# Performance work log

Measured on AMD Instinct MI355X. Metric: run time of the kernel, lower is better.

## Reference

```python
import jax, jax.numpy as jnp
import numpy as np

N = 40000
E = 640000
D = 256
H = 8
DH = D // H
DFF = 4 * D
SCALE = D ** (-0.5)
EPS = 1e-5


def layernorm(x, g, b):
    mu = jnp.mean(x, axis=-1, keepdims=True)
    var = jnp.mean(jnp.square(x - mu), axis=-1, keepdims=True)
    return (x - mu) * jax.lax.rsqrt(var + EPS) * g + b


def setup_inputs() -> dict:
    key = jax.random.key(0)
    ks = jax.random.split(key, 12)
    inv = 1.0 / np.sqrt(D)
    invf = 1.0 / np.sqrt(DFF)
    return {
        "triplet_h": jax.random.normal(ks[0], (N, D), dtype=jnp.float32),
        "src": jax.random.randint(ks[1], (E,), 0, N, dtype=jnp.int32),
        "dst": jax.random.randint(ks[2], (E,), 0, N, dtype=jnp.int32),
        "Wqkv": jax.random.uniform(ks[3], (D, 3 * D), jnp.float32, -inv, inv),
        "bqkv": jax.random.uniform(ks[4], (3 * D,), jnp.float32, -inv, inv),
        "ln_attn_g": jnp.ones((D,), jnp.float32),
        "ln_attn_b": jnp.zeros((D,), jnp.float32),
        "ln_res_g": jnp.ones((D,), jnp.float32),
        "ln_res_b": jnp.zeros((D,), jnp.float32),
        "W_in": jax.random.uniform(ks[5], (D, DFF), jnp.float32, -inv, inv),
        "b_in": jax.random.uniform(ks[6], (DFF,), jnp.float32, -inv, inv),
        "W_out": jax.random.uniform(ks[7], (DFF, D), jnp.float32, -invf, invf),
        "b_out": jax.random.uniform(ks[8], (D,), jnp.float32, -invf, invf),
    }


def reference(triplet_h, src, dst, Wqkv, bqkv, ln_attn_g, ln_attn_b,
              ln_res_g, ln_res_b, W_in, b_in, W_out, b_out):
    n = triplet_h.shape[0]
    h = layernorm(triplet_h, ln_attn_g, ln_attn_b)
    qkv = (h @ Wqkv + bqkv).reshape(n, 3, H, DH)
    q = qkv[:, 0] * SCALE          # [N, H, DH]
    k = qkv[:, 1]
    v = qkv[:, 2]

    # per-edge attention logits: dot(Q_src, K_dst) per head -> [E, H]
    scores = jnp.einsum('ehd,ehd->eh', q[src], k[dst])
    # segment softmax over incoming edges of each dst node
    m = jax.ops.segment_max(scores, dst, num_segments=n)      # [N, H]
    e = jnp.exp(scores - m[dst])
    s = jax.ops.segment_sum(e, dst, num_segments=n)           # [N, H]
    sa = e / s[dst]                                           # [E, H]

    # weighted scatter-sum of src V into dst nodes
    he = (v[src] * sa[:, :, None]).reshape(-1, D)             # [E, D]
    agg = jax.ops.segment_sum(he, dst, num_segments=n)        # [N, D]

    # Residual block: x = triplet_h + agg; x + MLP(LN(x))
    x = triplet_h + agg
    y = layernorm(x, ln_res_g, ln_res_b)
    y = jax.nn.gelu(y @ W_in + b_in, approximate=False) @ W_out + b_out
    return x + y
```

## Files before the change

kernel.cpp:

```cpp
#include <hip/hip_runtime.h>
#include <math.h>

#define N_NODES 40000
#define M_PAD   40064
#define N_EDGES 640000
#define D       256
#define H       8
#define DFF     1024
#define D3      768
#define ATT_SCALE 0.0625f
#define LN_EPS  1e-5f

typedef __attribute__((ext_vector_type(8))) short short8;
typedef __attribute__((ext_vector_type(4))) float f32x4;
typedef __attribute__((ext_vector_type(2))) float f32x2;

__device__ __forceinline__ unsigned short f2bf(float f) {
    unsigned int u = __builtin_bit_cast(unsigned int, f);
    u = (u + 0x7FFF + ((u >> 16) & 1)) >> 16;
    return (unsigned short)u;
}
__device__ __forceinline__ float bf2f(unsigned short u) {
    return __builtin_bit_cast(float, (unsigned int)u << 16);
}

__device__ __forceinline__ float fast_gelu(float x) {
    const float z  = fabsf(x) * 0.70710678118654752f;
    const float t  = __builtin_amdgcn_rcpf(1.0f + 0.3275911f * z);
    float p = 1.061405429f;
    p = p * t - 1.453152027f;
    p = p * t + 1.421413741f;
    p = p * t - 0.284496736f;
    p = p * t + 0.254829592f;
    const float e  = __expf(-z * z);
    const float ea = 1.0f - p * t * e;
    const float er = (x < 0.0f) ? -ea : ea;
    return 0.5f * x * (1.0f + er);
}

#define GLOAD_LDS16(g, l) \
    __builtin_amdgcn_global_load_lds((const __attribute__((address_space(1))) void*)(g), \
                                     (__attribute__((address_space(3))) void*)(l), 16, 0, 0)

#if __has_builtin(__builtin_amdgcn_cvt_pk_fp8_f32) && __has_builtin(__builtin_amdgcn_cvt_pk_f32_fp8)
#define HW_FP8 1
#else
#define HW_FP8 0
__device__ __forceinline__ unsigned char enc_e4m3(float f) {
    unsigned int u = __builtin_bit_cast(unsigned int, f);
    unsigned int s = (u >> 24) & 0x80;
    float a = fabsf(f);
    if (a >= 0x1p-6f) {
        unsigned int bits = __builtin_bit_cast(unsigned int, a);
        unsigned int q = bits >> 20;
        unsigned int rem = bits & 0xFFFFFu;
        q += (rem > 0x80000u) || ((rem == 0x80000u) && (q & 1));
        q -= 960;
        if (q > 126) q = 126;
        return (unsigned char)(s | q);
    }
    float t = a * 512.0f;
    unsigned int r = (unsigned int)rintf(t);
    return (unsigned char)(s | r);
}
__device__ __forceinline__ float dec_e4m3(unsigned int v) {
    unsigned int em = v & 0x7f;
    float n = __builtin_bit_cast(float, (em << 20) + 0x3C000000u);
    float r = (em >= 8) ? n : (float)em * 0x1p-9f;
    return (v & 0x80) ? -r : r;
}
#endif

__device__ __forceinline__ unsigned int pack4_e4m3(float a, float b, float c, float d) {
#if HW_FP8
    unsigned int w = (unsigned int)__builtin_amdgcn_cvt_pk_fp8_f32(a, b, 0, false);
    w = (unsigned int)__builtin_amdgcn_cvt_pk_fp8_f32(c, d, (int)w, true);
    return w;
#else
    return (unsigned int)enc_e4m3(a) | ((unsigned int)enc_e4m3(b) << 8)
         | ((unsigned int)enc_e4m3(c) << 16) | ((unsigned int)enc_e4m3(d) << 24);
#endif
}
__device__ __forceinline__ void dec4_e4m3(unsigned int w, float& a, float& b, float& c, float& d) {
#if HW_FP8
    f32x2 lo = __builtin_amdgcn_cvt_pk_f32_fp8((int)w, false);
    f32x2 hi = __builtin_amdgcn_cvt_pk_f32_fp8((int)w, true);
    a = lo[0]; b = lo[1]; c = hi[0]; d = hi[1];
#else
    a = dec_e4m3(w & 0xff); b = dec_e4m3((w >> 8) & 0xff);
    c = dec_e4m3((w >> 16) & 0xff); d = dec_e4m3(w >> 24);
#endif
}

#define NB_LN   (M_PAD / 4)
#define NB_PACK 352
#define NB_HIST (N_EDGES / 256)

__device__ __forceinline__ void ln_body(const float* __restrict__ in,
                                        const float* __restrict__ g,
                                        const float* __restrict__ b,
                                        unsigned short* __restrict__ out, int blk)
{
    const int row  = blk * 4 + (threadIdx.x >> 6);
    const int lane = threadIdx.x & 63;
    const size_t off = (((size_t)(row >> 4) * (D / 8) + (lane >> 1)) * 16 + (row & 15)) * 8
                       + (lane & 1) * 4;
    if (row >= N_NODES) {
        ushort4 z = {0, 0, 0, 0};
        *reinterpret_cast<ushort4*>(out + off) = z;
        return;
    }
    const float4 v = *reinterpret_cast<const float4*>(in + (size_t)row * D + lane * 4);
    float s  = v.x + v.y + v.z + v.w;
    float s2 = v.x * v.x + v.y * v.y + v.z * v.z + v.w * v.w;
#pragma unroll
    for (int o = 32; o > 0; o >>= 1) {
        s  += __shfl_xor(s,  o, 64);
        s2 += __shfl_xor(s2, o, 64);
    }
    const float mu  = s * (1.0f / D);
    const float var = s2 * (1.0f / D) - mu * mu;
    const float rs  = rsqrtf(var + LN_EPS);
    const float4 gg = *reinterpret_cast<const float4*>(g + lane * 4);
    const float4 bb = *reinterpret_cast<const float4*>(b + lane * 4);
    ushort4 o4;
    o4.x = f2bf((v.x - mu) * rs * gg.x + bb.x);
    o4.y = f2bf((v.y - mu) * rs * gg.y + bb.y);
    o4.z = f2bf((v.z - mu) * rs * gg.z + bb.z);
    o4.w = f2bf((v.w - mu) * rs * gg.w + bb.w);
    *reinterpret_cast<ushort4*>(out + off) = o4;
}

template <int K, int N>
__device__ __forceinline__ void pack_body(const float* __restrict__ W,
                                          unsigned short* __restrict__ Wpk, int blk)
{
    const int idx = blk * 256 + threadIdx.x;
    const int ni  = idx & 15;
    const int kc  = (idx >> 4) % (K / 8);
    const int nt  = idx / (16 * (K / 8));
    const int n   = nt * 16 + ni;
    unsigned short o[8];
#pragma unroll
    for (int i = 0; i < 8; ++i)
        o[i] = f2bf(W[(size_t)(kc * 8 + i) * N + n]);
    *reinterpret_cast<short8*>(Wpk + (size_t)idx * 8) = *reinterpret_cast<short8*>(o);
}

__global__ __launch_bounds__(256) void prep_kernel(const float* __restrict__ triplet_h,
                                                   const float* __restrict__ ln_g,
                                                   const float* __restrict__ ln_b,
                                                   unsigned short* __restrict__ h_xn,
                                                   const float* __restrict__ Wqkv,
                                                   const float* __restrict__ W_in,
                                                   const float* __restrict__ W_out,
                                                   unsigned short* __restrict__ pq,
                                                   unsigned short* __restrict__ pi,
                                                   unsigned short* __restrict__ po,
                                                   const int* __restrict__ dst,
                                                   int* __restrict__ counts)
{
    const int b = blockIdx.x;
    if (b < NB_LN) {
        ln_body(triplet_h, ln_g, ln_b, h_xn, b);
    } else if (b < NB_LN + NB_PACK) {
        const int pb = b - NB_LN;
        if (pb < 96)       pack_body<D, D3 >(Wqkv, pq, pb);
        else if (pb < 224) pack_body<D, DFF>(W_in, pi, pb - 96);
        else               pack_body<DFF, D>(W_out, po, pb - 224);
    } else {
        const int i = (b - NB_LN - NB_PACK) * 256 + threadIdx.x;
        atomicAdd(&counts[dst[i]], 1);
    }
}

template <int EPI, int K, int N>
__global__ __launch_bounds__(256, 4) void mfma_gemm_kernel(const unsigned short* __restrict__ A,
                                                           const unsigned short* __restrict__ Bpk,
                                                           const float* __restrict__ bias,
                                                           void* __restrict__ Cout,
                                                           void* __restrict__ Cout2,
                                                           void* __restrict__ Cout3,
                                                           const float* __restrict__ Xadd)
{
    constexpr int C = N / 128;
    constexpr int P = M_PAD / 128;

    const int bid = blockIdx.x;
    const int xcd = bid & 7;
    const int t   = bid >> 3;
    const int c   = t % C;
    const int p   = (t / C) * 8 + xcd;
    if (p >= P) return;

    __shared__ unsigned short As[4096];
    __shared__ unsigned short Bs[4096];

    const int tid  = threadIdx.x;
    const int wave = tid >> 6;
    const int lane = tid & 63;
    const int row0 = p * 128;
    const int col0 = c * 128;
    const int wm   = (wave >> 1) * 64;
    const int wn   = (wave & 1) * 64;
    const int g    = lane >> 4;
    const int q    = lane & 15;

    f32x4 acc[4][4] = {};

    const int fragoff = g * 128 + q * 8;

    for (int k0 = 0; k0 < K; k0 += 32) {
        const int kq = k0 >> 3;
#pragma unroll
        for (int cc = 0; cc < 2; ++cc) {
            const int mt = wave * 2 + cc;
            const unsigned short* gA =
                A + ((size_t)(row0 / 16 + mt) * (K / 8) + kq) * 128 + lane * 8;
            GLOAD_LDS16(gA, &As[mt * 512]);
            const unsigned short* gB =
                Bpk + ((size_t)(col0 / 16 + mt) * (K / 8) + kq) * 128 + lane * 8;
            GLOAD_LDS16(gB, &Bs[mt * 512]);
        }
        __syncthreads();

        short8 af[4], bf[4];
#pragma unroll
        for (int i = 0; i < 4; ++i) {
            af[i] = *reinterpret_cast<const short8*>(&As[(wm / 16 + i) * 512 + fragoff]);
            bf[i] = *reinterpret_cast<const short8*>(&Bs[(wn / 16 + i) * 512 + fragoff]);
        }
#pragma unroll
        for (int i = 0; i < 4; ++i)
#pragma unroll
            for (int j = 0; j < 4; ++j)
                acc[i][j] = __builtin_amdgcn_mfma_f32_16x16x32_bf16(bf[j], af[i], acc[i][j], 0, 0, 0);
        __syncthreads();
    }

    if constexpr (EPI == 0) {
        if (col0 < 256) {
            unsigned char* q8 = (unsigned char*)Cout;
#pragma unroll
            for (int j = 0; j < 4; ++j) {
                const int nb = col0 + wn + j * 16 + g * 4;
                const float4 bz = *reinterpret_cast<const float4*>(bias + nb);
#pragma unroll
                for (int i = 0; i < 4; ++i) {
                    const int r = row0 + wm + i * 16 + q;
                    if (r >= N_NODES) continue;
                    const unsigned int w = pack4_e4m3(acc[i][j][0] + bz.x, acc[i][j][1] + bz.y,
                                                      acc[i][j][2] + bz.z, acc[i][j][3] + bz.w);
                    *reinterpret_cast<unsigned int*>(q8 + (size_t)r * 256 + nb) = w;
                }
            }
        } else if (col0 < 512) {
            unsigned short* kb = (unsigned short*)Cout2;
#pragma unroll
            for (int j = 0; j < 4; ++j) {
                const int nb = col0 + wn + j * 16 + g * 4;
                const float4 bz = *reinterpret_cast<const float4*>(bias + nb);
#pragma unroll
                for (int i = 0; i < 4; ++i) {
                    const int r = row0 + wm + i * 16 + q;
                    if (r >= N_NODES) continue;
                    ushort4 u;
                    u.x = f2bf(acc[i][j][0] + bz.x);
                    u.y = f2bf(acc[i][j][1] + bz.y);
                    u.z = f2bf(acc[i][j][2] + bz.z);
                    u.w = f2bf(acc[i][j][3] + bz.w);
                    *reinterpret_cast<ushort4*>(kb + (size_t)r * 256 + (nb - 256)) = u;
                }
            }
        } else {
            unsigned char* v8 = (unsigned char*)Cout3;
#pragma unroll
            for (int j = 0; j < 4; ++j) {
                const int nb = col0 + wn + j * 16 + g * 4;
                const float4 bz = *reinterpret_cast<const float4*>(bias + nb);
#pragma unroll
                for (int i = 0; i < 4; ++i) {
                    const int r = row0 + wm + i * 16 + q;
                    if (r >= N_NODES) continue;
                    const unsigned int w = pack4_e4m3(acc[i][j][0] + bz.x, acc[i][j][1] + bz.y,
                                                      acc[i][j][2] + bz.z, acc[i][j][3] + bz.w);
                    *reinterpret_cast<unsigned int*>(v8 + (size_t)r * 256 + (nb - 512)) = w;
                }
            }
        }
    } else if constexpr (EPI == 1) {
#pragma unroll
        for (int j = 0; j < 4; ++j) {
            const int nb = col0 + wn + j * 16 + g * 4;
            const float4 bz = *reinterpret_cast<const float4*>(bias + nb);
#pragma unroll
            for (int i = 0; i < 4; ++i) {
                const int r = row0 + wm + i * 16 + q;
                const float o0 = fast_gelu(acc[i][j][0] + bz.x);
                const float o1 = fast_gelu(acc[i][j][1] + bz.y);
                const float o2 = fast_gelu(acc[i][j][2] + bz.z);
                const float o3 = fast_gelu(acc[i][j][3] + bz.w);
                const size_t off = (((size_t)(r >> 4) * (N / 8) + (nb >> 3)) * 16
                                    + (r & 15)) * 8 + (nb & 7);
                ushort4 u;
                u.x = f2bf(o0); u.y = f2bf(o1); u.z = f2bf(o2); u.w = f2bf(o3);
                *reinterpret_cast<ushort4*>((unsigned short*)Cout + off) = u;
            }
        }
    } else {
#pragma unroll
        for (int j = 0; j < 4; ++j) {
            const int nb = col0 + wn + j * 16 + g * 4;
            const float4 bz = *reinterpret_cast<const float4*>(bias + nb);
#pragma unroll
            for (int i = 0; i < 4; ++i) {
                const int r = row0 + wm + i * 16 + q;
                if (r >= N_NODES) continue;
                const f32x4 xd = __builtin_nontemporal_load(
                    reinterpret_cast<const f32x4*>(Xadd + (size_t)r * N + nb));
                f32x4 ov;
                ov[0] = acc[i][j][0] + bz.x + xd[0];
                ov[1] = acc[i][j][1] + bz.y + xd[1];
                ov[2] = acc[i][j][2] + bz.z + xd[2];
                ov[3] = acc[i][j][3] + bz.w + xd[3];
                __builtin_nontemporal_store(ov,
                    reinterpret_cast<f32x4*>((float*)Cout + (size_t)r * N + nb));
            }
        }
    }
}

__global__ __launch_bounds__(1024) void scan_kernel(const int* __restrict__ counts,
                                                    int* __restrict__ rowptr,
                                                    int* __restrict__ cursor)
{
    const int PER = 40;
    const int tid  = threadIdx.x;
    const int base = tid * PER;
    const bool act = (base < N_NODES);
    int s = 0;
    if (act) {
#pragma unroll
        for (int i = 0; i < PER / 4; ++i) {
            const int4 c4 = *reinterpret_cast<const int4*>(counts + base + i * 4);
            s += (c4.x + c4.y) + (c4.z + c4.w);
        }
    }
    __shared__ int sm[1024];
    sm[tid] = s;
    __syncthreads();
    for (int off = 1; off < 1024; off <<= 1) {
        int t = (tid >= off) ? sm[tid - off] : 0;
        __syncthreads();
        sm[tid] += t;
        __syncthreads();
    }
    int run = sm[tid] - s;
    if (act) {
#pragma unroll
        for (int i = 0; i < PER / 4; ++i) {
            const int4 c4 = *reinterpret_cast<const int4*>(counts + base + i * 4);
            int4 r4;
            r4.x = run;
            r4.y = r4.x + c4.x;
            r4.z = r4.y + c4.y;
            r4.w = r4.z + c4.z;
            run  = r4.w + c4.w;
            *reinterpret_cast<int4*>(rowptr + base + i * 4) = r4;
            *reinterpret_cast<int4*>(cursor + base + i * 4) = r4;
        }
    }
    if (tid == 1023) rowptr[N_NODES] = sm[1023];
}

__global__ __launch_bounds__(256) void fill_kernel(const int* __restrict__ src,
                                                   const int* __restrict__ dst,
                                                   int* __restrict__ cursor,
                                                   int* __restrict__ srcs)
{
    const int e = blockIdx.x * 256 + threadIdx.x;
    const int pos = atomicAdd(&cursor[dst[e]], 1);
    if (pos >= 0 && pos < N_EDGES) srcs[pos] = src[e];
}

__global__ __launch_bounds__(256) void fused_attn_kernel(const unsigned char* __restrict__ qf8,
                                                         const unsigned short* __restrict__ kbf,
                                                         const unsigned char* __restrict__ vf8,
                                                         const int* __restrict__ srcs,
                                                         const int* __restrict__ rowptr,
                                                         const float* __restrict__ triplet_h,
                                                         const float* __restrict__ g,
                                                         const float* __restrict__ b,
                                                         float* __restrict__ x,
                                                         unsigned short* __restrict__ xn)
{
    const int node = blockIdx.x * 4 + (threadIdx.x >> 6);
    const int lane = threadIdx.x & 63;
    int beg = rowptr[node];
    int end = rowptr[node + 1];
    beg = max(0, min(beg, N_EDGES));
    end = max(beg, min(end, N_EDGES));
    const int deg = end - beg;

    const ushort4 ku = *reinterpret_cast<const ushort4*>(
        kbf + (size_t)node * 256 + lane * 4);
    const float k0 = bf2f(ku.x) * ATT_SCALE, k1 = bf2f(ku.y) * ATT_SCALE;
    const float k2 = bf2f(ku.z) * ATT_SCALE, k3 = bf2f(ku.w) * ATT_SCALE;

    float dsum = 0.0f;
    float4 acc = {0.0f, 0.0f, 0.0f, 0.0f};

    for (int base = 0; base < deg; base += 64) {
        const int cnt = min(64, deg - base);
        const int idx = base + lane;
        const int sv = (idx < deg) ? srcs[beg + idx] : 0;
        int j = 0;
        for (; j + 4 <= cnt; j += 4) {
            const int s0 = __builtin_amdgcn_readlane(sv, j);
            const int s1 = __builtin_amdgcn_readlane(sv, j + 1);
            const int s2 = __builtin_amdgcn_readlane(sv, j + 2);
            const int s3 = __builtin_amdgcn_readlane(sv, j + 3);
            const unsigned int qa = *reinterpret_cast<const unsigned int*>(qf8 + (size_t)s0 * 256 + lane * 4);
            const unsigned int qb = *reinterpret_cast<const unsigned int*>(qf8 + (size_t)s1 * 256 + lane * 4);
            const unsigned int qc = *reinterpret_cast<const unsigned int*>(qf8 + (size_t)s2 * 256 + lane * 4);
            const unsigned int qd = *reinterpret_cast<const unsigned int*>(qf8 + (size_t)s3 * 256 + lane * 4);
            const unsigned int va = *reinterpret_cast<const unsigned int*>(vf8 + (size_t)s0 * 256 + lane * 4);
            const unsigned int vb = *reinterpret_cast<const unsigned int*>(vf8 + (size_t)s1 * 256 + lane * 4);
            const unsigned int vc = *reinterpret_cast<const unsigned int*>(vf8 + (size_t)s2 * 256 + lane * 4);
            const unsigned int vd = *reinterpret_cast<const unsigned int*>(vf8 + (size_t)s3 * 256 + lane * 4);
            float a0, a1, a2, a3;
            dec4_e4m3(qa, a0, a1, a2, a3);
            float p0 = a0 * k0 + a1 * k1 + a2 * k2 + a3 * k3;
            dec4_e4m3(qb, a0, a1, a2, a3);
            float p1 = a0 * k0 + a1 * k1 + a2 * k2 + a3 * k3;
            dec4_e4m3(qc, a0, a1, a2, a3);
            float p2 = a0 * k0 + a1 * k1 + a2 * k2 + a3 * k3;
            dec4_e4m3(qd, a0, a1, a2, a3);
            float p3 = a0 * k0 + a1 * k1 + a2 * k2 + a3 * k3;
            p0 += __shfl_xor(p0, 1, 64); p1 += __shfl_xor(p1, 1, 64);
            p2 += __shfl_xor(p2, 1, 64); p3 += __shfl_xor(p3, 1, 64);
            p0 += __shfl_xor(p0, 2, 64); p1 += __shfl_xor(p1, 2, 64);
            p2 += __shfl_xor(p2, 2, 64); p3 += __shfl_xor(p3, 2, 64);
            p0 += __shfl_xor(p0, 4, 64); p1 += __shfl_xor(p1, 4, 64);
            p2 += __shfl_xor(p2, 4, 64); p3 += __shfl_xor(p3, 4, 64);
            const float w0 = __expf(p0), w1 = __expf(p1), w2 = __expf(p2), w3 = __expf(p3);
            float v0, v1, v2, v3;
            dec4_e4m3(va, v0, v1, v2, v3);
            acc.x += w0 * v0; acc.y += w0 * v1; acc.z += w0 * v2; acc.w += w0 * v3;
            dec4_e4m3(vb, v0, v1, v2, v3);
            acc.x += w1 * v0; acc.y += w1 * v1; acc.z += w1 * v2; acc.w += w1 * v3;
            dec4_e4m3(vc, v0, v1, v2, v3);
            acc.x += w2 * v0; acc.y += w2 * v1; acc.z += w2 * v2; acc.w += w2 * v3;
            dec4_e4m3(vd, v0, v1, v2, v3);
            acc.x += w3 * v0; acc.y += w3 * v1; acc.z += w3 * v2; acc.w += w3 * v3;
            dsum += (w0 + w1) + (w2 + w3);
        }
        for (; j < cnt; ++j) {
            const int s0 = __builtin_amdgcn_readlane(sv, j);
            const unsigned int qa = *reinterpret_cast<const unsigned int*>(qf8 + (size_t)s0 * 256 + lane * 4);
            const unsigned int va = *reinterpret_cast<const unsigned int*>(vf8 + (size_t)s0 * 256 + lane * 4);
            float a0, a1, a2, a3;
            dec4_e4m3(qa, a0, a1, a2, a3);
            float p0 = a0 * k0 + a1 * k1 + a2 * k2 + a3 * k3;
            p0 += __shfl_xor(p0, 1, 64);
            p0 += __shfl_xor(p0, 2, 64);
            p0 += __shfl_xor(p0, 4, 64);
            const float w0 = __expf(p0);
            float v0, v1, v2, v3;
            dec4_e4m3(va, v0, v1, v2, v3);
            acc.x += w0 * v0; acc.y += w0 * v1; acc.z += w0 * v2; acc.w += w0 * v3;
            dsum += w0;
        }
    }
    const float inv = (deg > 0) ? 1.0f / dsum : 0.0f;

    const float4 th = *reinterpret_cast<const float4*>(
        triplet_h + (size_t)node * D + lane * 4);
    float4 xv;
    xv.x = th.x + acc.x * inv;
    xv.y = th.y + acc.y * inv;
    xv.z = th.z + acc.z * inv;
    xv.w = th.w + acc.w * inv;
    *reinterpret_cast<float4*>(x + (size_t)node * D + lane * 4) = xv;

    float s  = xv.x + xv.y + xv.z + xv.w;
    float s2 = xv.x * xv.x + xv.y * xv.y + xv.z * xv.z + xv.w * xv.w;
#pragma unroll
    for (int o = 32; o > 0; o >>= 1) {
        s  += __shfl_xor(s,  o, 64);
        s2 += __shfl_xor(s2, o, 64);
    }
    const float mu  = s * (1.0f / D);
    const float var = s2 * (1.0f / D) - mu * mu;
    const float rs  = rsqrtf(var + LN_EPS);
    const float4 gg = *reinterpret_cast<const float4*>(g + lane * 4);
    const float4 bb = *reinterpret_cast<const float4*>(b + lane * 4);
    ushort4 o4;
    o4.x = f2bf((xv.x - mu) * rs * gg.x + bb.x);
    o4.y = f2bf((xv.y - mu) * rs * gg.y + bb.y);
    o4.z = f2bf((xv.z - mu) * rs * gg.z + bb.z);
    o4.w = f2bf((xv.w - mu) * rs * gg.w + bb.w);
    const size_t off = (((size_t)(node >> 4) * (D / 8) + (lane >> 1)) * 16 + (node & 15)) * 8
                       + (lane & 1) * 4;
    *reinterpret_cast<ushort4*>(xn + off) = o4;
}

extern "C" void kernel_launch(void* const* d_in, const int* in_sizes, int n_in,
                              void* d_out, int out_size, void* d_ws, size_t ws_size,
                              hipStream_t stream)
{
    const float* triplet_h = (const float*)d_in[0];
    const int*   src       = (const int*)d_in[1];
    const int*   dst       = (const int*)d_in[2];
    const float* Wqkv      = (const float*)d_in[3];
    const float* bqkv      = (const float*)d_in[4];
    const float* ln_attn_g = (const float*)d_in[5];
    const float* ln_attn_b = (const float*)d_in[6];
    const float* ln_res_g  = (const float*)d_in[7];
    const float* ln_res_b  = (const float*)d_in[8];
    const float* W_in      = (const float*)d_in[9];
    const float* b_in      = (const float*)d_in[10];
    const float* W_out     = (const float*)d_in[11];
    const float* b_out     = (const float*)d_in[12];
    float* out = (float*)d_out;

    char* w = (char*)d_ws;
    unsigned short* bufA = (unsigned short*)w;
    w += (size_t)M_PAD * DFF * sizeof(unsigned short);
    unsigned short* h_xn = (unsigned short*)w;  w += (size_t)M_PAD * D * sizeof(unsigned short);
    float*          x    = (float*)w;           w += (size_t)N_NODES * D * sizeof(float);
    unsigned char*  qf8  = (unsigned char*)w;   w += (size_t)N_NODES * 256;
    unsigned char*  vf8  = (unsigned char*)w;   w += (size_t)N_NODES * 256;
    unsigned short* Wqkv_pk = (unsigned short*)w; w += (size_t)D * D3 * sizeof(unsigned short);
    unsigned short* Win_pk  = (unsigned short*)w; w += (size_t)D * DFF * sizeof(unsigned short);
    unsigned short* Wout_pk = (unsigned short*)w; w += (size_t)DFF * D * sizeof(unsigned short);
    int* counts = (int*)w;  w += (size_t)N_NODES * sizeof(int);
    int* rowptr = (int*)w;  w += (size_t)(N_NODES + 1) * sizeof(int);
    int* cursor = (int*)w;  w += (size_t)N_NODES * sizeof(int);
    int* srcs   = (int*)w;  w += (size_t)N_EDGES * sizeof(int);

    unsigned short* kbf = bufA;
    unsigned short* a1  = bufA;

    (void)hipMemsetAsync(counts, 0, (size_t)N_NODES * sizeof(int), stream);
    prep_kernel<<<NB_LN + NB_PACK + NB_HIST, 256, 0, stream>>>(
        triplet_h, ln_attn_g, ln_attn_b, h_xn,
        Wqkv, W_in, W_out, Wqkv_pk, Win_pk, Wout_pk, dst, counts);
    scan_kernel<<<1, 1024, 0, stream>>>(counts, rowptr, cursor);
    fill_kernel<<<N_EDGES / 256, 256, 0, stream>>>(src, dst, cursor, srcs);

    mfma_gemm_kernel<0, D, D3><<<((M_PAD / 128 + 7) / 8) * 8 * (D3 / 128), 256, 0, stream>>>(
        h_xn, Wqkv_pk, bqkv, qf8, kbf, vf8, nullptr);
    fused_attn_kernel<<<N_NODES / 4, 256, 0, stream>>>(qf8, kbf, vf8, srcs, rowptr, triplet_h,
                                                       ln_res_g, ln_res_b, x, h_xn);
    mfma_gemm_kernel<1, D, DFF><<<((M_PAD / 128 + 7) / 8) * 8 * (DFF / 128), 256, 0, stream>>>(
        h_xn, Win_pk, b_in, a1, nullptr, nullptr, nullptr);
    mfma_gemm_kernel<2, DFF, D><<<((M_PAD / 128 + 7) / 8) * 8 * (D / 128), 256, 0, stream>>>(
        a1, Wout_pk, b_out, out, nullptr, nullptr, x);

    (void)in_sizes; (void)n_in; (void)out_size; (void)ws_size;
}
```

Before: 377.5 us.

## Fold CSR scan into QKV GEMM and fill via histogram ranks

The histogram pass now records each edge's rank from its atomicAdd return value. The fill kernel then computes positions as rowptr+rank with no second round of atomics, which also removes the cursor array. The standalone single-block scan kernel is dropped, and its work moves into one extra block appended to the QKV GEMM launch. This saves a kernel launch and lets the scan overlap with GEMM work, at the cost of storing an E-sized rank array. The 256-thread scan with 160 elements per thread also serialises more work per thread.

```diff
diff --git a/kernel.cpp b/kernel.cpp
--- a/kernel.cpp
+++ b/kernel.cpp
@@ -158,7 +158,8 @@
                                                    unsigned short* __restrict__ pi,
                                                    unsigned short* __restrict__ po,
                                                    const int* __restrict__ dst,
-                                                   int* __restrict__ counts)
+                                                   int* __restrict__ counts,
+                                                   int* __restrict__ rank)
 {
     const int b = blockIdx.x;
     if (b < NB_LN) {
@@ -170,7 +171,7 @@
         else               pack_body<DFF, D>(W_out, po, pb - 224);
     } else {
         const int i = (b - NB_LN - NB_PACK) * 256 + threadIdx.x;
-        atomicAdd(&counts[dst[i]], 1);
+        rank[i] = atomicAdd(&counts[dst[i]], 1);
     }
 }
 
@@ -181,12 +182,58 @@
                                                            void* __restrict__ Cout,
                                                            void* __restrict__ Cout2,
                                                            void* __restrict__ Cout3,
-                                                           const float* __restrict__ Xadd)
-{
-    constexpr int C = N / 128;
-    constexpr int P = M_PAD / 128;
+                                                           const float* __restrict__ Xadd,
+                                                           const int* __restrict__ sc_counts,
+                                                           int* __restrict__ sc_rowptr)
+{
+    constexpr int C     = N / 128;
+    constexpr int P     = M_PAD / 128;
+    constexpr int NBLK0 = ((P + 7) / 8) * 8 * C;
 
     const int bid = blockIdx.x;
+
+    if constexpr (EPI == 0) {
+        if (bid == NBLK0) {
+            const int PER = 160;
+            const int tid  = threadIdx.x;
+            const int base = tid * PER;
+            const bool act = (base < N_NODES);
+            int s = 0;
+            if (act) {
+#pragma unroll
+                for (int i = 0; i < PER / 4; ++i) {
+                    const int4 c4 = *reinterpret_cast<const int4*>(sc_counts + base + i * 4);
+                    s += (c4.x + c4.y) + (c4.z + c4.w);
+                }
+            }
+            __shared__ int sm2[256];
+            sm2[tid] = s;
+            __syncthreads();
+            for (int off = 1; off < 256; off <<= 1) {
+                int t = (tid >= off) ? sm2[tid - off] : 0;
+                __syncthreads();
+                sm2[tid] += t;
+                __syncthreads();
+            }
+            int run = sm2[tid] - s;
+            if (act) {
+#pragma unroll
+                for (int i = 0; i < PER / 4; ++i) {
+                    const int4 c4 = *reinterpret_cast<const int4*>(sc_counts + base + i * 4);
+                    int4 r4;
+                    r4.x = run;
+                    r4.y = r4.x + c4.x;
+                    r4.z = r4.y + c4.y;
+                    r4.w = r4.z + c4.z;
+                    run  = r4.w + c4.w;
+                    *reinterpret_cast<int4*>(sc_rowptr + base + i * 4) = r4;
+                }
+            }
+            if (tid == 255) sc_rowptr[N_NODES] = sm2[255];
+            return;
+        }
+    }
+
     const int xcd = bid & 7;
     const int t   = bid >> 3;
     const int c   = t % C;
@@ -330,57 +377,15 @@
     }
 }
 
-__global__ __launch_bounds__(1024) void scan_kernel(const int* __restrict__ counts,
-                                                    int* __restrict__ rowptr,
-                                                    int* __restrict__ cursor)
-{
-    const int PER = 40;
-    const int tid  = threadIdx.x;
-    const int base = tid * PER;
-    const bool act = (base < N_NODES);
-    int s = 0;
-    if (act) {
-#pragma unroll
-        for (int i = 0; i < PER / 4; ++i) {
-            const int4 c4 = *reinterpret_cast<const int4*>(counts + base + i * 4);
-            s += (c4.x + c4.y) + (c4.z + c4.w);
-        }
-    }
-    __shared__ int sm[1024];
-    sm[tid] = s;
-    __syncthreads();
-    for (int off = 1; off < 1024; off <<= 1) {
-        int t = (tid >= off) ? sm[tid - off] : 0;
-        __syncthreads();
-        sm[tid] += t;
-        __syncthreads();
-    }
-    int run = sm[tid] - s;
-    if (act) {
-#pragma unroll
-        for (int i = 0; i < PER / 4; ++i) {
-            const int4 c4 = *reinterpret_cast<const int4*>(counts + base + i * 4);
-            int4 r4;
-            r4.x = run;
-            r4.y = r4.x + c4.x;
-            r4.z = r4.y + c4.y;
-            r4.w = r4.z + c4.z;
-            run  = r4.w + c4.w;
-            *reinterpret_cast<int4*>(rowptr + base + i * 4) = r4;
-            *reinterpret_cast<int4*>(cursor + base + i * 4) = r4;
-        }
-    }
-    if (tid == 1023) rowptr[N_NODES] = sm[1023];
-}
-
 __global__ __launch_bounds__(256) void fill_kernel(const int* __restrict__ src,
                                                    const int* __restrict__ dst,
-                                                   int* __restrict__ cursor,
+                                                   const int* __restrict__ rowptr,
+                                                   const int* __restrict__ rank,
                                                    int* __restrict__ srcs)
 {
     const int e = blockIdx.x * 256 + threadIdx.x;
-    const int pos = atomicAdd(&cursor[dst[e]], 1);
-    if (pos >= 0 && pos < N_EDGES) srcs[pos] = src[e];
+    const int pos = rowptr[dst[e]] + rank[e];
+    if ((unsigned)pos < N_EDGES) srcs[pos] = src[e];
 }
 
 __global__ __launch_bounds__(256) void fused_attn_kernel(const unsigned char* __restrict__ qf8,
@@ -536,7 +541,7 @@
     unsigned short* Wout_pk = (unsigned short*)w; w += (size_t)DFF * D * sizeof(unsigned short);
     int* counts = (int*)w;  w += (size_t)N_NODES * sizeof(int);
     int* rowptr = (int*)w;  w += (size_t)(N_NODES + 1) * sizeof(int);
-    int* cursor = (int*)w;  w += (size_t)N_NODES * sizeof(int);
+    int* rank   = (int*)w;  w += (size_t)N_EDGES * sizeof(int);
     int* srcs   = (int*)w;  w += (size_t)N_EDGES * sizeof(int);
 
     unsigned short* kbf = bufA;
@@ -545,18 +550,20 @@
     (void)hipMemsetAsync(counts, 0, (size_t)N_NODES * sizeof(int), stream);
     prep_kernel<<<NB_LN + NB_PACK + NB_HIST, 256, 0, stream>>>(
         triplet_h, ln_attn_g, ln_attn_b, h_xn,
-        Wqkv, W_in, W_out, Wqkv_pk, Win_pk, Wout_pk, dst, counts);
-    scan_kernel<<<1, 1024, 0, stream>>>(counts, rowptr, cursor);
-    fill_kernel<<<N_EDGES / 256, 256, 0, stream>>>(src, dst, cursor, srcs);
-
-    mfma_gemm_kernel<0, D, D3><<<((M_PAD / 128 + 7) / 8) * 8 * (D3 / 128), 256, 0, stream>>>(
-        h_xn, Wqkv_pk, bqkv, qf8, kbf, vf8, nullptr);
+        Wqkv, W_in, W_out, Wqkv_pk, Win_pk, Wout_pk, dst, counts, rank);
+
+    mfma_gemm_kernel<0, D, D3><<<((M_PAD / 128 + 7) / 8) * 8 * (D3 / 128) + 1, 256, 0, stream>>>(
+        h_xn, Wqkv_pk, bqkv, qf8, kbf, vf8, nullptr, counts, rowptr);
+
+    fill_kernel<<<N_EDGES / 256, 256, 0, stream>>>(src, dst, rowptr, rank, srcs);
+
     fused_attn_kernel<<<N_NODES / 4, 256, 0, stream>>>(qf8, kbf, vf8, srcs, rowptr, triplet_h,
                                                        ln_res_g, ln_res_b, x, h_xn);
+
     mfma_gemm_kernel<1, D, DFF><<<((M_PAD / 128 + 7) / 8) * 8 * (DFF / 128), 256, 0, stream>>>(
-        h_xn, Win_pk, b_in, a1, nullptr, nullptr, nullptr);
+        h_xn, Win_pk, b_in, a1, nullptr, nullptr, nullptr, nullptr, nullptr);
     mfma_gemm_kernel<2, DFF, D><<<((M_PAD / 128 + 7) / 8) * 8 * (D / 128), 256, 0, stream>>>(
-        a1, Wout_pk, b_out, out, nullptr, nullptr, x);
+        a1, Wout_pk, b_out, out, nullptr, nullptr, x, nullptr, nullptr);
 
     (void)in_sizes; (void)n_in; (void)out_size; (void)ws_size;
 }
```

Result: faster. 346.6 us (-8.2%).
